# Kernel optimization log

Hardware: AMD Instinct MI355X
Metric: run time of the kernel (lower is better)

Reference implementation:

```python
import jax, jax.numpy as jnp
import numpy as np

CLAMP_MIN = 1e-30
DIAG_SCALE = 10.0


def _fast_cdist(x1, x2):
    # mean-center both by x1's row-mean (as in torch source)
    adjustment = x1.mean(axis=-2, keepdims=True)
    x1 = x1 - adjustment
    x2 = x2 - adjustment
    x1_norm = jnp.sum(x1 * x1, axis=-1, keepdims=True)  # [N,1]
    x2_norm = jnp.sum(x2 * x2, axis=-1, keepdims=True)  # [N,1]
    # matmul trick: ||a-b||^2 = ||a||^2 + ||b||^2 - 2 a.b
    res = (-2.0) * (x1 @ x2.T) + x1_norm + x2_norm.T
    return jnp.sqrt(jnp.maximum(res, CLAMP_MIN))


def reference(x):
    # L2-normalize rows
    norm = jnp.linalg.norm(x, axis=-1, keepdims=True)
    x_norm = x / norm
    dist_mat = _fast_cdist(x_norm, x_norm)  # [N, N]
    d = jnp.diagonal(dist_mat)
    dist_mat = dist_mat + DIAG_SCALE * jnp.diag(1.0 - d)
    loss = jnp.max(1.0 / dist_mat, axis=1)
    return jnp.mean(loss)


def setup_inputs() -> dict:
    key = jax.random.key(0)
    x = jax.random.normal(key, (8192, 256), dtype=jnp.float32)
    return {"x": x}
```

## Files before the change

### kernel.cpp

```cpp
#include <hip/hip_runtime.h>
#include <stdint.h>

#define N_ROWS 8192
#define N_DIM  256
#define NB     64
#define NTRI   2080

typedef __attribute__((ext_vector_type(8))) short bf16x8;
typedef __attribute__((ext_vector_type(4))) float f32x4;

__device__ inline unsigned short f2bf(float f) {
    unsigned u = __float_as_uint(f);
    unsigned r = (u + 0x7FFFu + ((u >> 16) & 1u)) >> 16;
    return (unsigned short)r;
}
__device__ inline float bf2f(unsigned short b) {
    return __uint_as_float(((unsigned)b) << 16);
}
__device__ inline unsigned encf(float f) {
    unsigned u = __float_as_uint(f);
    return u ^ ((u & 0x80000000u) ? 0xFFFFFFFFu : 0x80000000u);
}
__device__ inline float decf(unsigned e) {
    unsigned u = e ^ ((e & 0x80000000u) ? 0x80000000u : 0xFFFFFFFFu);
    return __uint_as_float(u);
}
#define ENC_BIG 0xF149F2CAu

__global__ __launch_bounds__(256) void k_norm(const float* x,
                                              char* zb, long zstride,
                                              char* nsqb, long nstride,
                                              char* rminb, long rstride,
                                              float* out) {
    if (blockIdx.x == 0 && threadIdx.x == 0) *out = 0.0f;
    const int lane = threadIdx.x & 63;
    const int w    = threadIdx.x >> 6;
    const int row  = blockIdx.x * 4 + w;
    const float4* xr = (const float4*)(x + (size_t)row * N_DIM);
    float4 v = xr[lane];
    float ss = v.x*v.x + v.y*v.y + v.z*v.z + v.w*v.w;
    #pragma unroll
    for (int m = 1; m < 64; m <<= 1) ss += __shfl_xor(ss, m, 64);
    const float inv = 1.0f / sqrtf(ss);
    unsigned short b0 = f2bf(v.x * inv);
    unsigned short b1 = f2bf(v.y * inv);
    unsigned short b2 = f2bf(v.z * inv);
    unsigned short b3 = f2bf(v.w * inv);
    ushort4 uv; uv.x = b0; uv.y = b1; uv.z = b2; uv.w = b3;
    *(ushort4*)(zb + (size_t)row * zstride + lane * 8) = uv;
    float z0 = bf2f(b0), z1 = bf2f(b1), z2 = bf2f(b2), z3 = bf2f(b3);
    float s2 = z0*z0 + z1*z1 + z2*z2 + z3*z3;
    #pragma unroll
    for (int m = 1; m < 64; m <<= 1) s2 += __shfl_xor(s2, m, 64);
    if (lane == 0) {
        *(float*)(nsqb + (size_t)row * nstride) = s2;
        *(unsigned*)(rminb + (size_t)row * rstride) = ENC_BIG;
    }
}

#define GLD_LDS16(g, l)                                                        \
    __builtin_amdgcn_global_load_lds(                                          \
        (const __attribute__((address_space(1))) unsigned int*)(g),            \
        (__attribute__((address_space(3))) unsigned int*)(l), 16, 0, 0)

__global__ __launch_bounds__(256, 4) void k_gemm(const char* zb, long zstride,
                                                 const char* nsqb, long nstride,
                                                 char* rminb, long rstride) {
    __shared__ unsigned short As[128 * 64];
    __shared__ unsigned short Bs[128 * 64];
    __shared__ float pminR[128][2];
    __shared__ float pminC[128][2];

    const int tid   = threadIdx.x;
    const int lane  = tid & 63;
    const int w     = tid >> 6;
    const int waveM = (w >> 1) * 64;
    const int waveN = (w & 1) * 64;

    const int t = blockIdx.x;
    int br = (int)((129.0f - sqrtf(16641.0f - 8.0f * (float)t)) * 0.5f);
    while ((br + 1) * (129 - (br + 1)) / 2 <= t) ++br;
    while (br * (129 - br) / 2 > t) --br;
    const int bc = br + (t - br * (129 - br) / 2);
    const bool isdiag = (br == bc);

    const char* gA = zb + (size_t)br * 128 * zstride;
    const char* gB = zb + (size_t)bc * 128 * zstride;

    f32x4 acc[4][4];
    #pragma unroll
    for (int m = 0; m < 4; ++m)
        #pragma unroll
        for (int n = 0; n < 4; ++n)
            acc[m][n] = (f32x4){0.f, 0.f, 0.f, 0.f};

    for (int kk = 0; kk < 4; ++kk) {
        __syncthreads();
        #pragma unroll
        for (int c = 0; c < 4; ++c) {
            const int f    = c * 4096 + tid * 16;
            const int row  = f >> 7;
            const int slot = (f >> 4) & 7;
            const int c_g  = slot ^ (row & 7);
            GLD_LDS16(gA + (size_t)row * zstride + kk * 128 + c_g * 16,
                      (char*)As + c * 4096 + w * 1024);
            GLD_LDS16(gB + (size_t)row * zstride + kk * 128 + c_g * 16,
                      (char*)Bs + c * 4096 + w * 1024);
        }
        __syncthreads();

        #pragma unroll
        for (int s = 0; s < 2; ++s) {
            bf16x8 af[4], bfr[4];
            const int q = (lane >> 4) + s * 4;
            #pragma unroll
            for (int m = 0; m < 4; ++m) {
                const int rr = waveM + m * 16 + (lane & 15);
                af[m] = *(const bf16x8*)&As[rr * 64 + ((q ^ (rr & 7)) << 3)];
            }
            #pragma unroll
            for (int n = 0; n < 4; ++n) {
                const int rr = waveN + n * 16 + (lane & 15);
                bfr[n] = *(const bf16x8*)&Bs[rr * 64 + ((q ^ (rr & 7)) << 3)];
            }
            #pragma unroll
            for (int m = 0; m < 4; ++m)
                #pragma unroll
                for (int n = 0; n < 4; ++n)
                    acc[m][n] = __builtin_amdgcn_mfma_f32_16x16x32_bf16(af[m], bfr[n], acc[m][n], 0, 0, 0);
        }
    }

    asm volatile("" ::: "memory");

    float nj[4];
    #pragma unroll
    for (int n = 0; n < 4; ++n)
        nj[n] = *(const float*)(nsqb + (size_t)(bc * 128 + waveN + n * 16 + (lane & 15)) * nstride);

    float4 ni4[4];
    #pragma unroll
    for (int m = 0; m < 4; ++m) {
        const int row0 = br * 128 + waveM + m * 16 + (lane >> 4) * 4;
        if (nstride == 4) {
            ni4[m] = *(const float4*)(nsqb + (size_t)row0 * 4);
        } else {
            ni4[m].x = *(const float*)(nsqb + (size_t)(row0 + 0) * nstride);
            ni4[m].y = *(const float*)(nsqb + (size_t)(row0 + 1) * nstride);
            ni4[m].z = *(const float*)(nsqb + (size_t)(row0 + 2) * nstride);
            ni4[m].w = *(const float*)(nsqb + (size_t)(row0 + 3) * nstride);
        }
    }

    float rminv[4][4];
    float cminv[4];
    #pragma unroll
    for (int m = 0; m < 4; ++m)
        #pragma unroll
        for (int r = 0; r < 4; ++r)
            rminv[m][r] = 1e30f;
    #pragma unroll
    for (int n = 0; n < 4; ++n)
        cminv[n] = 1e30f;

    const int lrow0 = waveM + (lane >> 4) * 4;
    const int lcol0 = waveN + (lane & 15);
    #pragma unroll
    for (int m = 0; m < 4; ++m) {
        #pragma unroll
        for (int r = 0; r < 4; ++r) {
            const int lr = lrow0 + m * 16 + r;
            const float nir = ((const float*)&ni4[m])[r];
            #pragma unroll
            for (int n = 0; n < 4; ++n) {
                float u = fmaf(-2.0f, acc[m][n][r], nir + nj[n]);
                const bool diag = isdiag && (lr == (lcol0 + n * 16));
                u = diag ? 1e30f : u;
                rminv[m][r] = fminf(rminv[m][r], u);
                cminv[n]    = fminf(cminv[n], u);
            }
        }
    }
    #pragma unroll
    for (int mask = 1; mask < 16; mask <<= 1)
        #pragma unroll
        for (int m = 0; m < 4; ++m)
            #pragma unroll
            for (int r = 0; r < 4; ++r)
                rminv[m][r] = fminf(rminv[m][r], __shfl_xor(rminv[m][r], mask, 64));
    if ((lane & 15) == 0) {
        const int q = lane >> 4;
        #pragma unroll
        for (int m = 0; m < 4; ++m)
            #pragma unroll
            for (int r = 0; r < 4; ++r)
                pminR[waveM + m * 16 + q * 4 + r][w & 1] = rminv[m][r];
    }
    if (!isdiag) {
        #pragma unroll
        for (int mask = 16; mask < 64; mask <<= 1)
            #pragma unroll
            for (int n = 0; n < 4; ++n)
                cminv[n] = fminf(cminv[n], __shfl_xor(cminv[n], mask, 64));
        if (lane < 16) {
            #pragma unroll
            for (int n = 0; n < 4; ++n)
                pminC[waveN + n * 16 + lane][w >> 1] = cminv[n];
        }
    }
    __syncthreads();
    if (tid < 128) {
        const float v = fminf(pminR[tid][0], pminR[tid][1]);
        atomicMin((unsigned*)(rminb + (size_t)(br * 128 + tid) * rstride), encf(v));
        if (!isdiag) {
            const float vc = fminf(pminC[tid][0], pminC[tid][1]);
            atomicMin((unsigned*)(rminb + (size_t)(bc * 128 + tid) * rstride), encf(vc));
        }
    }
}

__global__ __launch_bounds__(256) void k_final(const char* nsqb, long nstride,
                                               const char* rminb, long rstride,
                                               float* out) {
    const int r = blockIdx.x * 256 + threadIdx.x;
    const float mn  = decf(*(const unsigned*)(rminb + (size_t)r * rstride));
    const float res = fmaxf(mn, 1e-30f);
    float loss = fmaxf(1.0f / sqrtf(res), 0.1f);
    #pragma unroll
    for (int m = 1; m < 64; m <<= 1) loss += __shfl_xor(loss, m, 64);
    __shared__ float wsum[4];
    const int lane = threadIdx.x & 63, w = threadIdx.x >> 6;
    if (lane == 0) wsum[w] = loss;
    __syncthreads();
    if (threadIdx.x == 0)
        atomicAdd(out, (wsum[0] + wsum[1] + wsum[2] + wsum[3]) * (1.0f / 8192.0f));
}

extern "C" void kernel_launch(void* const* d_in, const int* in_sizes, int n_in,
                              void* d_out, int out_size, void* d_ws, size_t ws_size,
                              hipStream_t stream) {
    float* x   = (float*)d_in[0];
    float* out = (float*)d_out;
    char*  ws  = (char*)d_ws;

    const size_t WS_NEED = 4u * 1024 * 1024 + 64 * 1024 + 4096;
    char *zb, *nsqb, *rminb;
    long zstride, nstride, rstride;
    if (ws_size >= WS_NEED) {
        zb    = ws;                                zstride = 512;
        nsqb  = ws + 4u * 1024 * 1024;             nstride = 4;
        rminb = ws + 4u * 1024 * 1024 + 32 * 1024; rstride = 4;
    } else {
        zb    = (char*)x;       zstride = 1024;
        nsqb  = (char*)x + 512; nstride = 1024;
        rminb = (char*)x + 516; rstride = 1024;
    }

    k_norm<<<N_ROWS / 4, 256, 0, stream>>>(x, zb, zstride, nsqb, nstride, rminb, rstride, out);
    k_gemm<<<NTRI, 256, 0, stream>>>(zb, zstride, nsqb, nstride, rminb, rstride);
    k_final<<<N_ROWS / 256, 256, 0, stream>>>(nsqb, nstride, rminb, rstride, out);
}
```

Baseline: 90.29 us.

## Pre-swizzle normalized matrix into MFMA fragment layout and drop LDS staging

```diff
diff --git a/kernel.cpp b/kernel.cpp
--- a/kernel.cpp
+++ b/kernel.cpp
@@ -27,11 +27,12 @@
 }
 #define ENC_BIG 0xF149F2CAu
 
-__global__ __launch_bounds__(256) void k_norm(const float* x,
-                                              char* zb, long zstride,
-                                              char* nsqb, long nstride,
-                                              char* rminb, long rstride,
-                                              float* out) {
+
+__global__ __launch_bounds__(256) void k_norm_fast(const float* __restrict__ x,
+                                                   char* __restrict__ zf,
+                                                   float* __restrict__ nsq,
+                                                   unsigned* __restrict__ rmin,
+                                                   float* __restrict__ out) {
     if (blockIdx.x == 0 && threadIdx.x == 0) *out = 0.0f;
     const int lane = threadIdx.x & 63;
     const int w    = threadIdx.x >> 6;
@@ -47,6 +48,162 @@
     unsigned short b2 = f2bf(v.z * inv);
     unsigned short b3 = f2bf(v.w * inv);
     ushort4 uv; uv.x = b0; uv.y = b1; uv.z = b2; uv.w = b3;
+    *(ushort4*)(zf + ((size_t)(row >> 4) << 13) + ((lane >> 1) << 8) +
+                ((row & 15) << 4) + ((lane & 1) << 3)) = uv;
+    float z0 = bf2f(b0), z1 = bf2f(b1), z2 = bf2f(b2), z3 = bf2f(b3);
+    float s2 = z0*z0 + z1*z1 + z2*z2 + z3*z3;
+    #pragma unroll
+    for (int m = 1; m < 64; m <<= 1) s2 += __shfl_xor(s2, m, 64);
+    if (lane == 0) {
+        nsq[row]  = s2;
+        rmin[row] = ENC_BIG;
+    }
+}
+
+__global__ __launch_bounds__(256, 3) void k_gemm_fast(const char* __restrict__ zf,
+                                                      const float* __restrict__ nsq,
+                                                      unsigned* __restrict__ rmin) {
+    __shared__ float pminR[128][2];
+    __shared__ float pminC[128][2];
+
+    const int tid   = threadIdx.x;
+    const int lane  = tid & 63;
+    const int w     = tid >> 6;
+    const int waveM = (w >> 1) * 64;
+    const int waveN = (w & 1) * 64;
+
+    const int t = blockIdx.x;
+    int br = (int)((129.0f - sqrtf(16641.0f - 8.0f * (float)t)) * 0.5f);
+    while ((br + 1) * (129 - (br + 1)) / 2 <= t) ++br;
+    while (br * (129 - br) / 2 > t) --br;
+    const int bc = br + (t - br * (129 - br) / 2);
+    const bool isdiag = (br == bc);
+
+    const int aBlk = br * 8 + (waveM >> 4);
+    const int bBlk = bc * 8 + (waveN >> 4);
+
+    f32x4 acc[4][4];
+    #pragma unroll
+    for (int m = 0; m < 4; ++m)
+        #pragma unroll
+        for (int n = 0; n < 4; ++n)
+            acc[m][n] = (f32x4){0.f, 0.f, 0.f, 0.f};
+
+    const char* laneA = zf + (size_t)aBlk * 8192 + lane * 16;
+    const char* laneB = zf + (size_t)bBlk * 8192 + lane * 16;
+
+    #pragma unroll
+    for (int s = 0; s < 8; ++s) {
+        bf16x8 af[4], bfr[4];
+        #pragma unroll
+        for (int m = 0; m < 4; ++m)
+            af[m] = *(const bf16x8*)(laneA + (size_t)m * 8192 + s * 1024);
+        #pragma unroll
+        for (int n = 0; n < 4; ++n)
+            bfr[n] = *(const bf16x8*)(laneB + (size_t)n * 8192 + s * 1024);
+        #pragma unroll
+        for (int m = 0; m < 4; ++m)
+            #pragma unroll
+            for (int n = 0; n < 4; ++n)
+                acc[m][n] = __builtin_amdgcn_mfma_f32_16x16x32_bf16(af[m], bfr[n], acc[m][n], 0, 0, 0);
+    }
+
+    asm volatile("" ::: "memory");
+
+    float nj[4];
+    #pragma unroll
+    for (int n = 0; n < 4; ++n)
+        nj[n] = nsq[bc * 128 + waveN + n * 16 + (lane & 15)];
+    float4 ni4[4];
+    #pragma unroll
+    for (int m = 0; m < 4; ++m)
+        ni4[m] = *(const float4*)&nsq[br * 128 + waveM + m * 16 + (lane >> 4) * 4];
+
+    float rminv[4][4];
+    float cminv[4];
+    #pragma unroll
+    for (int m = 0; m < 4; ++m)
+        #pragma unroll
+        for (int r = 0; r < 4; ++r)
+            rminv[m][r] = 1e30f;
+    #pragma unroll
+    for (int n = 0; n < 4; ++n)
+        cminv[n] = 1e30f;
+
+    const int lrow0 = waveM + (lane >> 4) * 4;
+    const int lcol0 = waveN + (lane & 15);
+    #pragma unroll
+    for (int m = 0; m < 4; ++m) {
+        #pragma unroll
+        for (int r = 0; r < 4; ++r) {
+            const int lr = lrow0 + m * 16 + r;
+            const float nir = ((const float*)&ni4[m])[r];
+            #pragma unroll
+            for (int n = 0; n < 4; ++n) {
+                float u = fmaf(-2.0f, acc[m][n][r], nir + nj[n]);
+                const bool diag = isdiag && (lr == (lcol0 + n * 16));
+                u = diag ? 1e30f : u;
+                rminv[m][r] = fminf(rminv[m][r], u);
+                cminv[n]    = fminf(cminv[n], u);
+            }
+        }
+    }
+    #pragma unroll
+    for (int mask = 1; mask < 16; mask <<= 1)
+        #pragma unroll
+        for (int m = 0; m < 4; ++m)
+            #pragma unroll
+            for (int r = 0; r < 4; ++r)
+                rminv[m][r] = fminf(rminv[m][r], __shfl_xor(rminv[m][r], mask, 64));
+    if ((lane & 15) == 0) {
+        const int q = lane >> 4;
+        #pragma unroll
+        for (int m = 0; m < 4; ++m)
+            #pragma unroll
+            for (int r = 0; r < 4; ++r)
+                pminR[waveM + m * 16 + q * 4 + r][w & 1] = rminv[m][r];
+    }
+    if (!isdiag) {
+        #pragma unroll
+        for (int mask = 16; mask < 64; mask <<= 1)
+            #pragma unroll
+            for (int n = 0; n < 4; ++n)
+                cminv[n] = fminf(cminv[n], __shfl_xor(cminv[n], mask, 64));
+        if (lane < 16) {
+            #pragma unroll
+            for (int n = 0; n < 4; ++n)
+                pminC[waveN + n * 16 + lane][w >> 1] = cminv[n];
+        }
+    }
+    __syncthreads();
+    if (tid < 128) {
+        const float v = fminf(pminR[tid][0], pminR[tid][1]);
+        atomicMin(&rmin[br * 128 + tid], encf(v));
+        if (!isdiag) {
+            const float vc = fminf(pminC[tid][0], pminC[tid][1]);
+            atomicMin(&rmin[bc * 128 + tid], encf(vc));
+        }
+    }
+}
+
+__global__ __launch_bounds__(256) void k_norm_fb(const float* x,
+                                                 char* zb, long zstride,
+                                                 char* nsqb, long nstride,
+                                                 char* rminb, long rstride,
+                                                 float* out) {
+    if (blockIdx.x == 0 && threadIdx.x == 0) *out = 0.0f;
+    const int lane = threadIdx.x & 63;
+    const int w    = threadIdx.x >> 6;
+    const int row  = blockIdx.x * 4 + w;
+    const float4* xr = (const float4*)(x + (size_t)row * N_DIM);
+    float4 v = xr[lane];
+    float ss = v.x*v.x + v.y*v.y + v.z*v.z + v.w*v.w;
+    #pragma unroll
+    for (int m = 1; m < 64; m <<= 1) ss += __shfl_xor(ss, m, 64);
+    const float inv = 1.0f / sqrtf(ss);
+    unsigned short b0 = f2bf(v.x * inv), b1 = f2bf(v.y * inv);
+    unsigned short b2 = f2bf(v.z * inv), b3 = f2bf(v.w * inv);
+    ushort4 uv; uv.x = b0; uv.y = b1; uv.z = b2; uv.w = b3;
     *(ushort4*)(zb + (size_t)row * zstride + lane * 8) = uv;
     float z0 = bf2f(b0), z1 = bf2f(b1), z2 = bf2f(b2), z3 = bf2f(b3);
     float s2 = z0*z0 + z1*z1 + z2*z2 + z3*z3;
@@ -63,9 +220,9 @@
         (const __attribute__((address_space(1))) unsigned int*)(g),            \
         (__attribute__((address_space(3))) unsigned int*)(l), 16, 0, 0)
 
-__global__ __launch_bounds__(256, 4) void k_gemm(const char* zb, long zstride,
-                                                 const char* nsqb, long nstride,
-                                                 char* rminb, long rstride) {
+__global__ __launch_bounds__(256, 4) void k_gemm_fb(const char* zb, long zstride,
+                                                    const char* nsqb, long nstride,
+                                                    char* rminb, long rstride) {
     __shared__ unsigned short As[128 * 64];
     __shared__ unsigned short Bs[128 * 64];
     __shared__ float pminR[128][2];
@@ -137,19 +294,14 @@
     #pragma unroll
     for (int n = 0; n < 4; ++n)
         nj[n] = *(const float*)(nsqb + (size_t)(bc * 128 + waveN + n * 16 + (lane & 15)) * nstride);
-
     float4 ni4[4];
     #pragma unroll
     for (int m = 0; m < 4; ++m) {
         const int row0 = br * 128 + waveM + m * 16 + (lane >> 4) * 4;
-        if (nstride == 4) {
-            ni4[m] = *(const float4*)(nsqb + (size_t)row0 * 4);
-        } else {
-            ni4[m].x = *(const float*)(nsqb + (size_t)(row0 + 0) * nstride);
-            ni4[m].y = *(const float*)(nsqb + (size_t)(row0 + 1) * nstride);
-            ni4[m].z = *(const float*)(nsqb + (size_t)(row0 + 2) * nstride);
-            ni4[m].w = *(const float*)(nsqb + (size_t)(row0 + 3) * nstride);
-        }
+        ni4[m].x = *(const float*)(nsqb + (size_t)(row0 + 0) * nstride);
+        ni4[m].y = *(const float*)(nsqb + (size_t)(row0 + 1) * nstride);
+        ni4[m].z = *(const float*)(nsqb + (size_t)(row0 + 2) * nstride);
+        ni4[m].w = *(const float*)(nsqb + (size_t)(row0 + 3) * nstride);
     }
 
     float rminv[4][4];
@@ -244,19 +396,20 @@
     char*  ws  = (char*)d_ws;
 
     const size_t WS_NEED = 4u * 1024 * 1024 + 64 * 1024 + 4096;
-    char *zb, *nsqb, *rminb;
-    long zstride, nstride, rstride;
     if (ws_size >= WS_NEED) {
-        zb    = ws;                                zstride = 512;
-        nsqb  = ws + 4u * 1024 * 1024;             nstride = 4;
-        rminb = ws + 4u * 1024 * 1024 + 32 * 1024; rstride = 4;
+        char*     zf   = ws;
+        float*    nsq  = (float*)(ws + 4u * 1024 * 1024);
+        unsigned* rmin = (unsigned*)(ws + 4u * 1024 * 1024 + 32 * 1024);
+        k_norm_fast<<<N_ROWS / 4, 256, 0, stream>>>(x, zf, nsq, rmin, out);
+        k_gemm_fast<<<NTRI, 256, 0, stream>>>(zf, nsq, rmin);
+        k_final<<<N_ROWS / 256, 256, 0, stream>>>((const char*)nsq, 4,
+                                                  (const char*)rmin, 4, out);
     } else {
-        zb    = (char*)x;       zstride = 1024;
-        nsqb  = (char*)x + 512; nstride = 1024;
-        rminb = (char*)x + 516; rstride = 1024;
-    }
-
-    k_norm<<<N_ROWS / 4, 256, 0, stream>>>(x, zb, zstride, nsqb, nstride, rminb, rstride, out);
-    k_gemm<<<NTRI, 256, 0, stream>>>(zb, zstride, nsqb, nstride, rminb, rstride);
-    k_final<<<N_ROWS / 256, 256, 0, stream>>>(nsqb, nstride, rminb, rstride, out);
-}
+        char* zb    = (char*)x;       long zstride = 1024;
+        char* nsqb  = (char*)x + 512; long nstride = 1024;
+        char* rminb = (char*)x + 516; long rstride = 1024;
+        k_norm_fb<<<N_ROWS / 4, 256, 0, stream>>>(x, zb, zstride, nsqb, nstride, rminb, rstride, out);
+        k_gemm_fb<<<NTRI, 256, 0, stream>>>(zb, zstride, nsqb, nstride, rminb, rstride);
+        k_final<<<N_ROWS / 256, 256, 0, stream>>>(nsqb, nstride, rminb, rstride, out);
+    }
+}
```

New measurement: 91.21 us. No clear change (+1.0%).
